# Kernel optimization log

Hardware: AMD Instinct MI355X
Metric: run time of the kernel (lower is better)

Reference implementation:

```python
import jax, jax.numpy as jnp
import numpy as np

N = 2048      # num graph nodes (activities + places)
D = 256       # embedding_size
C = 3 * D     # cat_embedding_size
V = 2         # num variants
L = 16        # activities per variant
E = 16 * N    # edges for the encoder GNN
DEG_P = 0.0156  # adjacency density (~32 out-degree)


def setup_inputs() -> dict:
    key = jax.random.key(0)
    ks = jax.random.split(key, 6)
    embeddings = jax.random.normal(ks[0], (N, D), dtype=jnp.float32)
    W_self = jax.random.normal(ks[1], (D, D), dtype=jnp.float32) * 0.05
    W_nbr = jax.random.normal(ks[2], (D, D), dtype=jnp.float32) * 0.05
    b = jnp.zeros((D,), dtype=jnp.float32)
    variants = jax.random.randint(ks[3], (V, L), 0, N, dtype=jnp.int32)
    original = (jax.random.uniform(ks[4], (N, N)) < DEG_P).astype(jnp.int32)
    edge_index = jax.random.randint(ks[5], (2, E), 0, N, dtype=jnp.int32)
    return {"embeddings": embeddings, "W_self": W_self, "W_nbr": W_nbr, "b": b,
            "variants": variants, "original": original, "edge_index": edge_index}


def _forward(embeddings, W_self, W_nbr, b, variants, original, edge_index):
    n, d = embeddings.shape
    c = 3 * d
    dt = embeddings.dtype
    adj = original.astype(dt)              # [N,N]; adj[i,j]=1 iff edge i->j (forward star = row)
    src_e, dst_e = edge_index[0], edge_index[1]

    def encoder(x):
        # SecondEncoder approximated as one GCN-style message-passing layer
        msg = jax.ops.segment_sum(x[src_e], dst_e, num_segments=n)
        return jax.nn.relu(x @ W_self + msg @ W_nbr + b)

    def run_variant(acts):  # acts: [L] int32
        onehot = jax.nn.one_hot(acts, n, dtype=dt)                # [L,N]
        incl = jnp.flip(jnp.cumsum(jnp.flip(onehot, 0), 0), 0)    # sum_{j>=i} onehot[j]
        present_later = ((incl - onehot) > 0).astype(dt)          # set of nodes in acts[i+1:]

        def step(carry, inp):
            emb, pi, summary = carry
            a, plater = inp
            followers = adj[a]                                    # forward star of activity a
            has = jnp.any(followers > 0)
            adj_m = adj * plater[None, :]                         # edges into later-in-variant activities
            dest_cnt = adj_m.sum(axis=1)                          # |destination set| per candidate place
            dst_all = adj_m @ emb                                 # summed destination embeddings, [N,D]
            mask = jnp.where(has, ((followers > 0) & (dest_cnt > 0)).astype(dt), 0.0)
            # cat = (place_f, src_f, dst_f) per considered place
            cat = jnp.concatenate(
                [emb, jnp.broadcast_to(emb[a][None, :], emb.shape), dst_all], axis=1) * mask[:, None]
            pi = pi + cat                                         # places_info[place] += cat
            # prev_embedding_summary += places_info[place] for each considered place
            summary = summary + (mask[:, None] * pi).sum(axis=0)
            # places_info[considered] += prev_embedding_summary
            pi = pi + mask[:, None] * summary[None, :]
            emb = jnp.where(has, encoder(emb), emb)               # encoder skipped when no followers
            return (emb, pi, summary), None

        init = (embeddings, jnp.zeros((n, c), dt), jnp.zeros((c,), dt))
        (_, pi, _), _ = jax.lax.scan(step, init, (acts, present_later))
        return pi

    # variant shuffle in the original is irrelevant: embeddings reset each variant
    # and final_places_info is a sum over variants.
    return jax.vmap(run_variant)(variants).sum(axis=0)


def reference(embeddings, W_self, W_nbr, b, variants, original, edge_index):
    return _forward(embeddings, W_self, W_nbr, b, variants, original, edge_index)
```

## Files before the change

kernel.cpp:

```cpp
#include <hip/hip_runtime.h>

#define N 2048
#define D 256
#define C 768
#define V 2
#define L 16
#define NSTATE 15
#define NAPP 14
#define TCAP 256
#define FCAP 64

typedef __attribute__((ext_vector_type(8))) short bf16x8;
typedef __attribute__((ext_vector_type(4))) float f32x4;

__device__ __forceinline__ ushort bf16_rn(float x) {
  unsigned u = __float_as_uint(x);
  u += 0x7FFFu + ((u >> 16) & 1u);
  return (ushort)(u >> 16);
}
__device__ __forceinline__ float bf16_f(ushort h) {
  return __uint_as_float(((unsigned)h) << 16);
}

__device__ __forceinline__ size_t a_addr(int row, int k) {
  return ((size_t)(row >> 5) * 4 + (k >> 6)) * 2048 + (row & 31) * 64 + (k & 63);
}
__device__ __forceinline__ size_t wt_addr(int n, int k) {
  return ((size_t)(n >> 5) * 4 + (k >> 6)) * 2048 + (n & 31) * 64 + (k & 63);
}

__global__ __launch_bounds__(256) void k_init(
    const float* __restrict__ emb, const float* __restrict__ Ws,
    const float* __restrict__ Wn, float* __restrict__ states0,
    ushort* __restrict__ WtHi, ushort* __restrict__ WtLo,
    ushort* __restrict__ A0hi, ushort* __restrict__ A0lo,
    float* __restrict__ out, int* __restrict__ fillpos) {
  size_t i = (size_t)blockIdx.x * 256 + threadIdx.x;
  size_t stride = (size_t)gridDim.x * 256;
  for (size_t x = i; x < (size_t)N * D; x += stride) {
    float v = emb[x];
    states0[x] = v;
    ushort h = bf16_rn(v);
    ushort l = bf16_rn(v - bf16_f(h));
    size_t a = a_addr((int)(x >> 8), (int)(x & 255));
    A0hi[a] = h;
    A0lo[a] = l;
  }
  for (size_t x = i; x < (size_t)512 * 256; x += stride) {
    int n = (int)(x >> 8), k = (int)(x & 255);
    float v = (n < 256) ? Ws[(size_t)k * 256 + n] : Wn[(size_t)k * 256 + (n - 256)];
    ushort h = bf16_rn(v);
    size_t a = wt_addr(n, k);
    WtHi[a] = h;
    WtLo[a] = bf16_rn(v - bf16_f(h));
  }
  for (size_t x = i; x < (size_t)N * C; x += stride) out[x] = 0.f;
  for (size_t x = i; x < N; x += stride) fillpos[x] = 0;
}

__global__ __launch_bounds__(256) void k_degA(
    const int* __restrict__ ei, int E, int* __restrict__ fillpos,
    const int* __restrict__ adj, const int* __restrict__ variants,
    int* __restrict__ stepP, int* __restrict__ stepDm,
    int* __restrict__ stepCnt, int* __restrict__ hasG, int* __restrict__ tlG) {
  __shared__ int tl_sh[16];
  __shared__ int foll[FCAP], fbits[FCAP];
  __shared__ int sh_tc, sh_fcnt, sh_ecnt;
  int t = threadIdx.x;
  if (blockIdx.x < 128) {
    for (int e = blockIdx.x * 256 + t; e < E; e += 128 * 256)
      atomicAdd(&fillpos[ei[E + e]], 1);
    return;
  }
  int vi = blockIdx.x - 128;
  int v = vi / L, i = vi % L;
  int a = variants[vi];
  if (t == 0) {
    int cnt = 0;
    for (int j = i + 1; j < L; j++) {
      int x = variants[v * L + j];
      bool dup = false;
      for (int q = 0; q < cnt; q++) if (tl_sh[q] == x) dup = true;
      if (!dup) tl_sh[cnt++] = x;
    }
    sh_tc = cnt;
    sh_fcnt = 0;
    sh_ecnt = 0;
    for (int q = 0; q < cnt; q++) tlG[vi * 16 + q] = tl_sh[q];
  }
  __syncthreads();
  for (int p = t; p < N; p += 256) {
    if (adj[(size_t)a * N + p] != 0) {
      int f = atomicAdd(&sh_fcnt, 1);
      if (f < FCAP) foll[f] = p;
    }
  }
  __syncthreads();
  int fc = sh_fcnt < FCAP ? sh_fcnt : FCAP;
  int tc = sh_tc;
  for (int x = t; x < fc; x += 256) fbits[x] = 0;
  __syncthreads();
  for (int x = t; x < fc * tc; x += 256) {
    int fi = x / tc, q = x - fi * tc;
    if (adj[(size_t)foll[fi] * N + tl_sh[q]] != 0) atomicOr(&fbits[fi], 1 << q);
  }
  __syncthreads();
  for (int fi = t; fi < fc; fi += 256) {
    int bits = fbits[fi];
    if (bits) {
      int e = atomicAdd(&sh_ecnt, 1);
      stepP[vi * FCAP + e] = foll[fi];
      stepDm[vi * FCAP + e] = bits;
    }
  }
  __syncthreads();
  if (t == 0) {
    stepCnt[vi] = sh_ecnt;
    hasG[vi] = (sh_fcnt > 0);
  }
}

__global__ __launch_bounds__(256) void k_scan(int* __restrict__ fillpos,
                                              int* __restrict__ row_ptr) {
  __shared__ int part[256];
  __shared__ int base[257];
  int t = threadIdx.x;
  int v[8];
  int s = 0;
  for (int j = 0; j < 8; j++) { v[j] = fillpos[t * 8 + j]; s += v[j]; }
  part[t] = s;
  __syncthreads();
  if (t == 0) {
    int acc = 0;
    for (int q = 0; q < 256; q++) { base[q] = acc; acc += part[q]; }
    base[256] = acc;
  }
  __syncthreads();
  int acc = base[t];
  for (int j = 0; j < 8; j++) {
    row_ptr[t * 8 + j] = acc;
    fillpos[t * 8 + j] = acc;
    acc += v[j];
  }
  if (t == 255) row_ptr[N] = base[256];
}

__global__ __launch_bounds__(256) void k_fillB(
    const int* __restrict__ ei, int E, int* __restrict__ fillpos,
    int* __restrict__ csr_src,
    const int* __restrict__ stepP, const int* __restrict__ stepDm,
    const int* __restrict__ stepCnt, const int* __restrict__ hasG,
    int* __restrict__ entP, int* __restrict__ entPrev, int* __restrict__ entDm,
    int* __restrict__ offsG, int* __restrict__ kidxG, int* __restrict__ cmatG,
    int* __restrict__ lastPG, int* __restrict__ lastIG, int* __restrict__ lastMG,
    int* __restrict__ cntG) {
  __shared__ int pmask[N];
  __shared__ int sP[16][FCAP];
  __shared__ int sDm[16][FCAP];
  __shared__ int cnt[16], offs[17];
  __shared__ int cmat_sh[256];
  __shared__ int sh_u;
  int t = threadIdx.x;
  if (blockIdx.x < 128) {
    for (int e = blockIdx.x * 256 + t; e < E; e += 128 * 256) {
      int dst = ei[E + e];
      int pos = atomicAdd(&fillpos[dst], 1);
      csr_src[pos] = ei[e];
    }
    return;
  }
  int v = blockIdx.x - 128;
  for (int p = t; p < N; p += 256) pmask[p] = 0;
  for (int x = t; x < 256; x += 256) cmat_sh[x] = 0;
  if (t < 16) cnt[t] = stepCnt[v * L + t];
  if (t == 0) sh_u = 0;
  __syncthreads();
  if (t == 0) {
    int acc = 0;
    for (int i = 0; i < 16; i++) {
      offs[i] = acc < TCAP ? acc : TCAP;
      acc += cnt[i];
    }
    offs[16] = acc < TCAP ? acc : TCAP;
    cntG[v * 2 + 0] = offs[16];
    int k = 0;
    for (int i = 0; i < L; i++) {
      kidxG[v * 16 + i] = k;
      if (hasG[v * L + i]) k++;
    }
  }
  for (int x = t; x < 16 * FCAP; x += 256) {
    int i = x >> 6, f = x & 63;
    if (f < stepCnt[v * L + i]) {
      int p = stepP[(v * L + i) * FCAP + f];
      sP[i][f] = p;
      sDm[i][f] = stepDm[(v * L + i) * FCAP + f];
      atomicOr(&pmask[p], 1 << i);
    }
  }
  __syncthreads();
  for (int x = t; x < 16 * FCAP; x += 256) {
    int i = x >> 6, f = x & 63;
    if (f < cnt[i]) {
      int e = offs[i] + f;
      if (e < TCAP) {
        int p = sP[i][f];
        entP[v * TCAP + e] = p;
        entDm[v * TCAP + e] = sDm[i][f];
        int m = pmask[p] & ((1 << i) - 1);
        int prev = -1;
        if (m) {
          int j = 31 - __clz(m);
          int cj = cnt[j];
          for (int f2 = 0; f2 < cj; f2++)
            if (sP[j][f2] == p) { prev = offs[j] + f2; break; }
        }
        entPrev[v * TCAP + e] = prev;
      }
    }
  }
  __syncthreads();
  for (int p = t; p < N; p += 256) {
    int m = pmask[p];
    if (m) {
      int u = atomicAdd(&sh_u, 1);
      int j = 31 - __clz(m);
      int li = -1;
      int cj = cnt[j];
      for (int f2 = 0; f2 < cj; f2++)
        if (sP[j][f2] == p) { li = offs[j] + f2; break; }
      lastPG[v * TCAP + u] = p;
      lastIG[v * TCAP + u] = li;
      lastMG[v * TCAP + u] = m;
      int mm = m;
      while (mm) {
        int bi = __ffs(mm) - 1; mm &= mm - 1;
        int m2 = m & ((1 << bi) - 1);
        while (m2) {
          int bj = __ffs(m2) - 1; m2 &= m2 - 1;
          atomicAdd(&cmat_sh[bi * 16 + bj], 1);
        }
      }
    }
  }
  __syncthreads();
  if (t == 0) cntG[v * 2 + 1] = sh_u;
  for (int x = t; x < 256; x += 256) cmatG[v * 256 + x] = cmat_sh[x];
  for (int x = t; x < 17; x += 256) offsG[v * 17 + x] = offs[x];
}

__global__ __launch_bounds__(256) void k_gemm(
    const ushort* __restrict__ Ah, const ushort* __restrict__ Al,
    const ushort* __restrict__ Wh_g, const ushort* __restrict__ Wl_g,
    float* __restrict__ Z) {
  __shared__ __align__(16) ushort Ash[2][32][72], Asl[2][32][72];
  __shared__ __align__(16) ushort Wsh[2][32][72], Wsl[2][32][72];
  const int tid = threadIdx.x, wave = tid >> 6, lane = tid & 63;
  const int quad = lane >> 4, l16 = lane & 15;
  const int wr = wave >> 1, wc = wave & 1;
  const int mb = blockIdx.x, nb = blockIdx.y;
  const int sr = tid >> 3, sc = (tid & 7) * 8;

  f32x4 acc = {0.f, 0.f, 0.f, 0.f};
  size_t abase = (size_t)mb * 4 * 2048 + (size_t)tid * 8;
  size_t wbase = (size_t)nb * 4 * 2048 + (size_t)tid * 8;
  {
    uint4 ra  = *(const uint4*)&Ah[abase];
    uint4 rl  = *(const uint4*)&Al[abase];
    uint4 rwh = *(const uint4*)&Wh_g[wbase];
    uint4 rwl = *(const uint4*)&Wl_g[wbase];
    *(uint4*)&Ash[0][sr][sc] = ra;
    *(uint4*)&Asl[0][sr][sc] = rl;
    *(uint4*)&Wsh[0][sr][sc] = rwh;
    *(uint4*)&Wsl[0][sr][sc] = rwl;
  }
  __syncthreads();
#pragma unroll
  for (int c = 0; c < 4; c++) {
    const int rb = c & 1;
    uint4 ra, rl, rwh, rwl;
    if (c < 3) {
      size_t o = (size_t)(c + 1) * 2048;
      ra  = *(const uint4*)&Ah[abase + o];
      rl  = *(const uint4*)&Al[abase + o];
      rwh = *(const uint4*)&Wh_g[wbase + o];
      rwl = *(const uint4*)&Wl_g[wbase + o];
    }
#pragma unroll
    for (int kf = 0; kf < 2; kf++) {
      int ko = kf * 32 + quad * 8;
      bf16x8 a_h = *(const bf16x8*)&Ash[rb][wr * 16 + l16][ko];
      bf16x8 a_l = *(const bf16x8*)&Asl[rb][wr * 16 + l16][ko];
      bf16x8 w_h = *(const bf16x8*)&Wsh[rb][wc * 16 + l16][ko];
      bf16x8 w_l = *(const bf16x8*)&Wsl[rb][wc * 16 + l16][ko];
      acc = __builtin_amdgcn_mfma_f32_16x16x32_bf16(a_h, w_h, acc, 0, 0, 0);
      acc = __builtin_amdgcn_mfma_f32_16x16x32_bf16(a_h, w_l, acc, 0, 0, 0);
      acc = __builtin_amdgcn_mfma_f32_16x16x32_bf16(a_l, w_h, acc, 0, 0, 0);
    }
    if (c < 3) {
      const int wb = rb ^ 1;
      *(uint4*)&Ash[wb][sr][sc] = ra;
      *(uint4*)&Asl[wb][sr][sc] = rl;
      *(uint4*)&Wsh[wb][sr][sc] = rwh;
      *(uint4*)&Wsl[wb][sr][sc] = rwl;
      __syncthreads();
    }
  }
  int col = nb * 32 + wc * 16 + l16;
  int row0 = mb * 32 + wr * 16 + quad * 4;
#pragma unroll
  for (int r = 0; r < 4; r++)
    Z[(size_t)(row0 + r) * 512 + col] = acc[r];
}

__global__ __launch_bounds__(256) void k_comb(
    const float* __restrict__ Z, const float* __restrict__ bias,
    const int* __restrict__ row_ptr, const int* __restrict__ csr_src,
    float* __restrict__ stnext, ushort* __restrict__ NAh,
    ushort* __restrict__ NAl) {
  int row = blockIdx.x * 4 + (threadIdx.x >> 6);
  int lane = threadIdx.x & 63;
  const float4* Zp = (const float4*)Z;
  float4 acc = Zp[(size_t)row * 128 + lane];
  float4 acc2 = {0.f, 0.f, 0.f, 0.f};
  float4 acc3 = {0.f, 0.f, 0.f, 0.f};
  float4 acc4 = {0.f, 0.f, 0.f, 0.f};
  int e0 = row_ptr[row], e1 = row_ptr[row + 1];
  int e = e0;
  for (; e + 3 < e1; e += 4) {
    int s0 = csr_src[e], s1 = csr_src[e + 1];
    int s2 = csr_src[e + 2], s3 = csr_src[e + 3];
    float4 x0 = Zp[(size_t)s0 * 128 + 64 + lane];
    float4 x1 = Zp[(size_t)s1 * 128 + 64 + lane];
    float4 x2 = Zp[(size_t)s2 * 128 + 64 + lane];
    float4 x3 = Zp[(size_t)s3 * 128 + 64 + lane];
    acc.x += x0.x; acc.y += x0.y; acc.z += x0.z; acc.w += x0.w;
    acc2.x += x1.x; acc2.y += x1.y; acc2.z += x1.z; acc2.w += x1.w;
    acc3.x += x2.x; acc3.y += x2.y; acc3.z += x2.z; acc3.w += x2.w;
    acc4.x += x3.x; acc4.y += x3.y; acc4.z += x3.z; acc4.w += x3.w;
  }
  for (; e < e1; e++) {
    float4 x0 = Zp[(size_t)csr_src[e] * 128 + 64 + lane];
    acc.x += x0.x; acc.y += x0.y; acc.z += x0.z; acc.w += x0.w;
  }
  float4 bv = ((const float4*)bias)[lane];
  float v0 = fmaxf(acc.x + acc2.x + acc3.x + acc4.x + bv.x, 0.f);
  float v1 = fmaxf(acc.y + acc2.y + acc3.y + acc4.y + bv.y, 0.f);
  float v2 = fmaxf(acc.z + acc2.z + acc3.z + acc4.z + bv.z, 0.f);
  float v3 = fmaxf(acc.w + acc2.w + acc3.w + acc4.w + bv.w, 0.f);
  *(float4*)(stnext + (size_t)row * D + lane * 4) = make_float4(v0, v1, v2, v3);
  ushort h0 = bf16_rn(v0), h1 = bf16_rn(v1), h2 = bf16_rn(v2), h3 = bf16_rn(v3);
  size_t ca = a_addr(row, lane * 4);
  *(ushort4*)&NAh[ca] = make_ushort4(h0, h1, h2, h3);
  *(ushort4*)&NAl[ca] = make_ushort4(
      bf16_rn(v0 - bf16_f(h0)), bf16_rn(v1 - bf16_f(h1)),
      bf16_rn(v2 - bf16_f(h2)), bf16_rn(v3 - bf16_f(h3)));
}

#define PI_LDS_BYTES (TCAP * 64 * 4 + 16 * 64 * 4 + 16 * 64 * 4 + 256 * 4 + \
                      3 * TCAP * 4 + 17 * 4 + 16 * 4 + 256 * 4)
__global__ __launch_bounds__(256) void k_pi(
    const float* __restrict__ states, float* __restrict__ out,
    const int* __restrict__ variants,
    const int* __restrict__ entP, const int* __restrict__ entPrev,
    const int* __restrict__ entDm, const int* __restrict__ offsG,
    const int* __restrict__ kidxG, const int* __restrict__ tlG,
    const int* __restrict__ cmatG, const int* __restrict__ lastPG,
    const int* __restrict__ lastIG, const int* __restrict__ lastMG,
    const int* __restrict__ cntG) {
  extern __shared__ __align__(16) float smf[];
  float* catb = smf;
  float* S_lds = catb + TCAP * 64;
  float* aS = S_lds + 16 * 64;
  float* cmatf = aS + 16 * 64;
  int* eP  = (int*)(cmatf + 256);
  int* ePr = eP + TCAP;
  int* eDm = ePr + TCAP;
  int* offs = eDm + TCAP;
  int* kidx = offs + 17;
  int* tl = kidx + 16;
  int v = blockIdx.x / 12, cgi = blockIdx.x % 12;
  int grp = cgi >> 2;
  int tid = threadIdx.x, lane = tid & 63, w = tid >> 6;
  int cl = (cgi & 3) * 64 + lane;
  int col = cgi * 64 + lane;

  int T = cntG[v * 2 + 0], U = cntG[v * 2 + 1];
  for (int x = tid; x < T; x += 256) {
    eP[x] = entP[v * TCAP + x];
    ePr[x] = entPrev[v * TCAP + x];
    eDm[x] = entDm[v * TCAP + x];
  }
  for (int x = tid; x < 17; x += 256) offs[x] = offsG[v * 17 + x];
  if (tid < 16) kidx[tid] = kidxG[v * 16 + tid];
  for (int x = tid; x < 256; x += 256) {
    tl[x] = tlG[v * 256 + x];
    cmatf[x] = (float)cmatG[v * 256 + x];
  }
  __syncthreads();

  for (int i = 0; i < L; i++) {
    int kk = kidx[i]; if (kk > NSTATE - 1) kk = NSTATE - 1;
    const float* embS = states + (size_t)kk * N * D;
    int o0 = offs[i], o1 = offs[i + 1];
    if (grp == 0) {
      for (int e = o0 + w; e < o1; e += 4)
        catb[e * 64 + lane] = embS[(size_t)eP[e] * D + cl];
    } else if (grp == 1) {
      float embA = embS[(size_t)variants[v * L + i] * D + cl];
      for (int e = o0 + w; e < o1; e += 4) catb[e * 64 + lane] = embA;
    } else {
      for (int e = o0 + w; e < o1; e += 4) {
        float sa = 0.f;
        int bm = eDm[e];
        while (bm) {
          int q = __ffs(bm) - 1; bm &= bm - 1;
          sa += embS[(size_t)tl[i * 16 + q] * D + cl];
        }
        catb[e * 64 + lane] = sa;
      }
    }
  }
  __syncthreads();
  for (int u = w; u < U; u += 4) {
    int li = lastIG[v * TCAP + u];
    int len = 0;
    for (int c2 = li; c2 >= 0; c2 = ePr[c2]) len++;
    for (int j = 1; j < len; j++) {
      int c2 = li;
      for (int k = 0; k < len - 1 - j; k++) c2 = ePr[c2];
      catb[c2 * 64 + lane] += catb[ePr[c2] * 64 + lane];
    }
  }
  __syncthreads();
  for (int i = w; i < 16; i += 4) {
    float a = 0.f;
    for (int e = offs[i]; e < offs[i + 1]; e++) a += catb[e * 64 + lane];
    aS[i * 64 + lane] = a;
  }
  __syncthreads();
  if (w == 0) {
    float S[16];
    float Sp = 0.f;
#pragma unroll
    for (int i = 0; i < 16; i++) {
      float sv = Sp + aS[i * 64 + lane];
#pragma unroll
      for (int j = 0; j < 16; j++)
        if (j < i) sv += cmatf[i * 16 + j] * S[j];
      S[i] = sv;
      S_lds[i * 64 + lane] = sv;
      Sp = sv;
    }
  }
  __syncthreads();
  for (int u = w; u < U; u += 4) {
    int p = lastPG[v * TCAP + u];
    int li = lastIG[v * TCAP + u];
    int m = lastMG[v * TCAP + u];
    float acc = catb[li * 64 + lane];
    while (m) {
      int q = __ffs(m) - 1; m &= m - 1;
      acc += S_lds[q * 64 + lane];
    }
    atomicAdd(&out[(size_t)p * C + col], acc);
  }
}

extern "C" void kernel_launch(void* const* d_in, const int* in_sizes, int n_in,
                              void* d_out, int out_size, void* d_ws, size_t ws_size,
                              hipStream_t stream) {
  const float* emb      = (const float*)d_in[0];
  const float* Ws       = (const float*)d_in[1];
  const float* Wn       = (const float*)d_in[2];
  const float* bias     = (const float*)d_in[3];
  const int*   variants = (const int*)d_in[4];
  const int*   adj      = (const int*)d_in[5];
  const int*   ei       = (const int*)d_in[6];
  const int    E        = in_sizes[6] / 2;
  float* out            = (float*)d_out;

  char* base = (char*)d_ws;
  float* states = (float*)base;            base += (size_t)NSTATE * N * D * 4;
  float* Z      = (float*)base;            base += (size_t)N * 512 * 4;
  ushort* WtHi  = (ushort*)base;           base += (size_t)512 * 256 * 2;
  ushort* WtLo  = (ushort*)base;           base += (size_t)512 * 256 * 2;
  ushort* A0h   = (ushort*)base;           base += (size_t)N * D * 2;
  ushort* A0l   = (ushort*)base;           base += (size_t)N * D * 2;
  ushort* A1h   = (ushort*)base;           base += (size_t)N * D * 2;
  ushort* A1l   = (ushort*)base;           base += (size_t)N * D * 2;
  int* row_ptr  = (int*)base;              base += (N + 1) * 4;
  int* fillpos  = (int*)base;              base += N * 4;
  int* csr_src  = (int*)base;              base += (size_t)E * 4;
  int* stepP    = (int*)base;              base += V * L * FCAP * 4;
  int* stepDm   = (int*)base;              base += V * L * FCAP * 4;
  int* stepCnt  = (int*)base;              base += V * L * 4;
  int* hasG     = (int*)base;              base += V * L * 4;
  int* entP     = (int*)base;              base += V * TCAP * 4;
  int* entPrev  = (int*)base;              base += V * TCAP * 4;
  int* entDm    = (int*)base;              base += V * TCAP * 4;
  int* offsG    = (int*)base;              base += V * 17 * 4;
  int* kidxG    = (int*)base;              base += V * 16 * 4;
  int* tlG      = (int*)base;              base += V * 256 * 4;
  int* cmatG    = (int*)base;              base += V * 256 * 4;
  int* lastPG   = (int*)base;              base += V * TCAP * 4;
  int* lastIG   = (int*)base;              base += V * TCAP * 4;
  int* lastMG   = (int*)base;              base += V * TCAP * 4;
  int* cntG     = (int*)base;              base += V * 2 * 4;

  hipFuncSetAttribute((const void*)k_pi,
                      hipFuncAttributeMaxDynamicSharedMemorySize, PI_LDS_BYTES);

  k_init<<<512, 256, 0, stream>>>(emb, Ws, Wn, states, WtHi, WtLo, A0h, A0l,
                                  out, fillpos);
  k_degA<<<128 + V * L, 256, 0, stream>>>(ei, E, fillpos, adj, variants,
                                          stepP, stepDm, stepCnt, hasG, tlG);
  k_scan<<<1, 256, 0, stream>>>(fillpos, row_ptr);
  k_fillB<<<128 + V, 256, 0, stream>>>(ei, E, fillpos, csr_src, stepP, stepDm,
                                       stepCnt, hasG, entP, entPrev, entDm,
                                       offsG, kidxG, cmatG, lastPG, lastIG,
                                       lastMG, cntG);

  ushort* AH[2] = {A0h, A1h};
  ushort* AL[2] = {A0l, A1l};
  for (int s = 0; s < NAPP; s++) {
    int cur = s & 1, nxt = cur ^ 1;
    k_gemm<<<dim3(64, 16), 256, 0, stream>>>(AH[cur], AL[cur], WtHi, WtLo, Z);
    k_comb<<<N / 4, 256, 0, stream>>>(Z, bias, row_ptr, csr_src,
                                      states + (size_t)(s + 1) * N * D,
                                      AH[nxt], AL[nxt]);
  }
  k_pi<<<V * 12, 256, PI_LDS_BYTES, stream>>>(states, out, variants, entP,
                                              entPrev, entDm, offsG, kidxG, tlG,
                                              cmatG, lastPG, lastIG, lastMG,
                                              cntG);
}
```

Baseline: 346.2 us.

## Load weights into registers, stream A via direct global-to-LDS loads with swizzle

Rewrites the GEMM staging. Each wave now loads its weight fragments straight into registers instead of staging them through shared memory. A tiles are copied with global_load_lds direct-to-LDS transfers, and the global A layout gets an XOR swizzle so LDS reads avoid bank conflicts without padding. This removes the register round-trip for A and halves LDS traffic, at the cost of more registers. The synchronization around the async LDS loads also becomes more delicate.

```diff
diff --git a/kernel.cpp b/kernel.cpp
--- a/kernel.cpp
+++ b/kernel.cpp
@@ -23,10 +23,19 @@
 }
 
 __device__ __forceinline__ size_t a_addr(int row, int k) {
-  return ((size_t)(row >> 5) * 4 + (k >> 6)) * 2048 + (row & 31) * 64 + (k & 63);
+  size_t chunk = (size_t)(row >> 5) * 4 + (k >> 6);
+  int idx = (((row & 31) * 64 + (k & 63)) ^ ((row & 7) << 3));
+  return chunk * 2048 + idx;
 }
 __device__ __forceinline__ size_t wt_addr(int n, int k) {
   return ((size_t)(n >> 5) * 4 + (k >> 6)) * 2048 + (n & 31) * 64 + (k & 63);
+}
+
+__device__ __forceinline__ void gload16(const ushort* __restrict__ g,
+                                        ushort* l) {
+  __builtin_amdgcn_global_load_lds(
+      (const __attribute__((address_space(1))) void*)g,
+      (__attribute__((address_space(3))) void*)l, 16, 0, 0);
 }
 
 __global__ __launch_bounds__(256) void k_init(
@@ -253,61 +262,56 @@
     const ushort* __restrict__ Ah, const ushort* __restrict__ Al,
     const ushort* __restrict__ Wh_g, const ushort* __restrict__ Wl_g,
     float* __restrict__ Z) {
-  __shared__ __align__(16) ushort Ash[2][32][72], Asl[2][32][72];
-  __shared__ __align__(16) ushort Wsh[2][32][72], Wsl[2][32][72];
+  __shared__ __align__(16) ushort Ash[2][2048], Asl[2][2048];
   const int tid = threadIdx.x, wave = tid >> 6, lane = tid & 63;
   const int quad = lane >> 4, l16 = lane & 15;
   const int wr = wave >> 1, wc = wave & 1;
   const int mb = blockIdx.x, nb = blockIdx.y;
-  const int sr = tid >> 3, sc = (tid & 7) * 8;
+
+  bf16x8 wh[8], wl[8];
+  {
+    const int wrow = wc * 16 + l16;
+#pragma unroll
+    for (int u = 0; u < 8; u++) {
+      const int c = u >> 1, kf = u & 1;
+      const int ko = kf * 32 + quad * 8;
+      size_t idx = ((size_t)nb * 4 + c) * 2048 + wrow * 64 + ko;
+      wh[u] = *(const bf16x8*)&Wh_g[idx];
+      wl[u] = *(const bf16x8*)&Wl_g[idx];
+    }
+  }
+
+  const size_t abase = (size_t)mb * 4 * 2048;
+  gload16(&Ah[abase + tid * 8], &Ash[0][wave * 512]);
+  gload16(&Al[abase + tid * 8], &Asl[0][wave * 512]);
+  __syncthreads();
 
   f32x4 acc = {0.f, 0.f, 0.f, 0.f};
-  size_t abase = (size_t)mb * 4 * 2048 + (size_t)tid * 8;
-  size_t wbase = (size_t)nb * 4 * 2048 + (size_t)tid * 8;
-  {
-    uint4 ra  = *(const uint4*)&Ah[abase];
-    uint4 rl  = *(const uint4*)&Al[abase];
-    uint4 rwh = *(const uint4*)&Wh_g[wbase];
-    uint4 rwl = *(const uint4*)&Wl_g[wbase];
-    *(uint4*)&Ash[0][sr][sc] = ra;
-    *(uint4*)&Asl[0][sr][sc] = rl;
-    *(uint4*)&Wsh[0][sr][sc] = rwh;
-    *(uint4*)&Wsl[0][sr][sc] = rwl;
-  }
-  __syncthreads();
+  const int arow = wr * 16 + l16;
+  const int aswz = (arow & 7) << 3;
 #pragma unroll
   for (int c = 0; c < 4; c++) {
     const int rb = c & 1;
-    uint4 ra, rl, rwh, rwl;
     if (c < 3) {
-      size_t o = (size_t)(c + 1) * 2048;
-      ra  = *(const uint4*)&Ah[abase + o];
-      rl  = *(const uint4*)&Al[abase + o];
-      rwh = *(const uint4*)&Wh_g[wbase + o];
-      rwl = *(const uint4*)&Wl_g[wbase + o];
+      size_t o = abase + (size_t)(c + 1) * 2048 + tid * 8;
+      gload16(&Ah[o], &Ash[rb ^ 1][wave * 512]);
+      gload16(&Al[o], &Asl[rb ^ 1][wave * 512]);
     }
 #pragma unroll
     for (int kf = 0; kf < 2; kf++) {
-      int ko = kf * 32 + quad * 8;
-      bf16x8 a_h = *(const bf16x8*)&Ash[rb][wr * 16 + l16][ko];
-      bf16x8 a_l = *(const bf16x8*)&Asl[rb][wr * 16 + l16][ko];
-      bf16x8 w_h = *(const bf16x8*)&Wsh[rb][wc * 16 + l16][ko];
-      bf16x8 w_l = *(const bf16x8*)&Wsl[rb][wc * 16 + l16][ko];
-      acc = __builtin_amdgcn_mfma_f32_16x16x32_bf16(a_h, w_h, acc, 0, 0, 0);
-      acc = __builtin_amdgcn_mfma_f32_16x16x32_bf16(a_h, w_l, acc, 0, 0, 0);
-      acc = __builtin_amdgcn_mfma_f32_16x16x32_bf16(a_l, w_h, acc, 0, 0, 0);
-    }
-    if (c < 3) {
-      const int wb = rb ^ 1;
-      *(uint4*)&Ash[wb][sr][sc] = ra;
-      *(uint4*)&Asl[wb][sr][sc] = rl;
-      *(uint4*)&Wsh[wb][sr][sc] = rwh;
-      *(uint4*)&Wsl[wb][sr][sc] = rwl;
-      __syncthreads();
-    }
-  }
-  int col = nb * 32 + wc * 16 + l16;
-  int row0 = mb * 32 + wr * 16 + quad * 4;
+      const int ko = kf * 32 + quad * 8;
+      const int aidx = (arow * 64 + ko) ^ aswz;
+      bf16x8 a_h = *(const bf16x8*)&Ash[rb][aidx];
+      bf16x8 a_l = *(const bf16x8*)&Asl[rb][aidx];
+      const int u = c * 2 + kf;
+      acc = __builtin_amdgcn_mfma_f32_16x16x32_bf16(a_h, wh[u], acc, 0, 0, 0);
+      acc = __builtin_amdgcn_mfma_f32_16x16x32_bf16(a_h, wl[u], acc, 0, 0, 0);
+      acc = __builtin_amdgcn_mfma_f32_16x16x32_bf16(a_l, wh[u], acc, 0, 0, 0);
+    }
+    if (c < 3) __syncthreads();
+  }
+  const int col = nb * 32 + wc * 16 + l16;
+  const int row0 = mb * 32 + wr * 16 + quad * 4;
 #pragma unroll
   for (int r = 0; r < 4; r++)
     Z[(size_t)(row0 + r) * 512 + col] = acc[r];
```

Result: slower. 416.6 us (+20.3%).
